# Kernel tuning notes

Measured on AMD Instinct MI355X. Metric: run time of the kernel, lower is better.

The kernel has to match this reference:

```python
import jax, jax.numpy as jnp
import numpy as np

P = 7          # output_size
SR = 2         # sampling_ratio
SCALES = (0.25, 0.125, 0.0625, 0.03125)
K_MIN, K_MAX = 2.0, 5.0   # -log2(max scale), -log2(min scale)
LVL0, S0, EPS = 4.0, 224.0, 1e-6  # torchvision LevelMapper defaults


def _coverage(x1, x2, size):
    """Fractional per-pixel coverage of interval [x1, x2] along an axis.
    Reproduces fill_masks_for_boxes edge weighting. x1, x2: [K] -> [K, size]."""
    cols = jnp.arange(size, dtype=x1.dtype)[None, :]
    x1f = jnp.floor(x1)[:, None]
    x2c = jnp.ceil(x2)[:, None]
    inside = ((cols >= x1f) & (cols < x2c)).astype(x1.dtype)
    wl = jnp.where(cols == x1f, 1.0 + x1f - x1[:, None], 1.0)
    wr = jnp.where(cols == x2c - 1.0, 1.0 + x2[:, None] - x2c, 1.0)
    return inside * wl * wr


def _axis_interp(coord, size):
    """torchvision roi_align (aligned=False) 1D bilinear setup.
    Returns lo/hi indices and weights (zeroed for out-of-range points)."""
    valid = ((coord >= -1.0) & (coord <= size)).astype(coord.dtype)
    c = jnp.maximum(coord, 0.0)
    lo0 = jnp.floor(c)
    top = lo0 >= size - 1
    lo = jnp.where(top, float(size - 1), lo0)
    hi = jnp.where(top, float(size - 1), lo0 + 1.0)
    c = jnp.where(top, float(size - 1), c)
    frac = c - lo
    return lo.astype(jnp.int32), hi.astype(jnp.int32), (1.0 - frac) * valid, frac * valid


def _level_roi(feat, scale, ub, bo, bidx):
    """Masked RoIAlign of the union box over one pyramid level.
    feat: [N,C,H,W]; ub, bo: [K,4] image-coord boxes; bidx: [K] int32."""
    N, C, H, W = feat.shape
    K = ub.shape[0]
    ubs = ub * scale
    bos = bo * scale

    def clipb(b):
        return (jnp.clip(b[:, 0], 0.0, W), jnp.clip(b[:, 1], 0.0, H),
                jnp.clip(b[:, 2], 0.0, W), jnp.clip(b[:, 3], 0.0, H))

    ux1, uy1, ux2, uy2 = clipb(ubs)
    ox1, oy1, ox2, oy2 = clipb(bos)
    # Separable pair-mask coverage (NOTE: torch code mutates boxes_h into the
    # union in-place before mask construction, so the 'h' mask is the union mask).
    cxu = _coverage(ux1, ux2, W)  # [K,W]
    cyu = _coverage(uy1, uy2, H)  # [K,H]
    cxo = _coverage(ox1, ox2, W)
    cyo = _coverage(oy1, oy2, H)

    x1, y1, x2, y2 = ubs[:, 0], ubs[:, 1], ubs[:, 2], ubs[:, 3]
    roi_w = jnp.maximum(x2 - x1, 1.0)
    roi_h = jnp.maximum(y2 - y1, 1.0)
    i = jnp.arange(P * SR)
    t = (i // SR).astype(jnp.float32) + ((i % SR).astype(jnp.float32) + 0.5) / SR  # bin units
    px = x1[:, None] + t[None, :] * (roi_w / P)[:, None]  # [K, P*SR]
    py = y1[:, None] + t[None, :] * (roi_h / P)[:, None]
    xlo, xhi, wxl, wxh = _axis_interp(px, W)
    ylo, yhi, wyl, wyh = _axis_interp(py, H)

    ga = lambda tab, idx: jnp.take_along_axis(tab, idx, axis=1)
    ys, wy = (ylo, yhi), (wyl, wyh)
    xs, wx = (xlo, xhi), (wxl, wxh)
    myu = (ga(cyu, ylo), ga(cyu, yhi))
    mxu = (ga(cxu, xlo), ga(cxu, xhi))
    myo = (ga(cyo, ylo), ga(cyo, yhi))
    mxo = (ga(cxo, xlo), ga(cxo, xhi))

    acc = jnp.zeros((K, P * SR, P * SR, C), dtype=feat.dtype)
    for a in range(2):
        for b in range(2):
            # gather corner features: [K, Ps, Ps, C]
            fv = feat[bidx[:, None, None], :, ys[a][:, :, None], xs[b][:, None, :]]
            m = jnp.maximum(myu[a][:, :, None] * mxu[b][:, None, :],
                            myo[a][:, :, None] * mxo[b][:, None, :])
            wgt = wy[a][:, :, None] * wx[b][:, None, :] * m
            acc = acc + wgt[..., None] * fv
    out = acc.reshape(K, P, SR, P, SR, C).mean(axis=(2, 4))  # avg over sample grid
    return jnp.transpose(out, (0, 3, 1, 2))  # [K, C, P, P]


def _forward(feat0, feat1, feat2, feat3, boxes_h, boxes_o):
    feats = (feat0, feat1, feat2, feat3)
    bidx = boxes_h[:, 0].astype(jnp.int32)
    bh = boxes_h[:, 1:]
    bo = boxes_o[:, 1:]
    ub = jnp.stack([jnp.minimum(bh[:, 0], bo[:, 0]), jnp.minimum(bh[:, 1], bo[:, 1]),
                    jnp.maximum(bh[:, 2], bo[:, 2]), jnp.maximum(bh[:, 3], bo[:, 3])], axis=1)
    # Level mapping (boxes_h already mutated into the union in the torch code)
    su = jnp.sqrt((ub[:, 2] - ub[:, 0]) * (ub[:, 3] - ub[:, 1]))
    so = jnp.sqrt((bo[:, 2] - bo[:, 0]) * (bo[:, 3] - bo[:, 1]))
    s = jnp.minimum(su, so)
    lv = (jnp.clip(jnp.floor(LVL0 + jnp.log2(s / S0 + EPS)), K_MIN, K_MAX)).astype(jnp.int32) - int(K_MIN)
    K, C = boxes_h.shape[0], feat0.shape[1]
    out = jnp.zeros((K, C, P, P), dtype=feat0.dtype)
    for l, (f, sc) in enumerate(zip(feats, SCALES)):
        ol = _level_roi(f, sc, ub, bo, bidx)
        out = out + jnp.where((lv == l)[:, None, None, None], ol, 0.0)
    return out


def setup_inputs() -> dict:
    key = jax.random.key(0)
    ks = jax.random.split(key, 12)
    feat0 = jax.random.normal(ks[0], (2, 256, 128, 128), dtype=jnp.float32)
    feat1 = jax.random.normal(ks[1], (2, 256, 64, 64), dtype=jnp.float32)
    feat2 = jax.random.normal(ks[2], (2, 256, 32, 32), dtype=jnp.float32)
    feat3 = jax.random.normal(ks[3], (2, 256, 16, 16), dtype=jnp.float32)
    K = 512
    bidx = jax.random.randint(ks[4], (K,), 0, 2).astype(jnp.float32)

    def mk(k):
        k1, k2, k3, k4 = jax.random.split(k, 4)
        x1 = jax.random.uniform(k1, (K,), minval=0.0, maxval=112.0)
        y1 = jax.random.uniform(k2, (K,), minval=0.0, maxval=112.0)
        w = jax.random.uniform(k3, (K,), minval=16.0, maxval=400.0)
        h = jax.random.uniform(k4, (K,), minval=16.0, maxval=400.0)
        return jnp.stack([bidx, x1, y1, x1 + w, y1 + h], axis=1)  # image is 512x512

    return {"feat0": feat0, "feat1": feat1, "feat2": feat2, "feat3": feat3,
            "boxes_h": mk(ks[5]), "boxes_o": mk(ks[6])}


def reference(feat0, feat1, feat2, feat3, boxes_h, boxes_o):
    return _forward(feat0, feat1, feat2, feat3, boxes_h, boxes_o)
```

## Files before the change

kernel.cpp:

```cpp
#include <hip/hip_runtime.h>
#include <math.h>

#define PP 7
#define CCH 256

__device__ __forceinline__ float coverage(float colf, float a, float b) {
    float af = floorf(a);
    float bc = ceilf(b);
    float v  = (colf >= af && colf < bc) ? 1.0f : 0.0f;
    float wl = (colf == af) ? (1.0f + af - a) : 1.0f;
    float wr = (colf == bc - 1.0f) ? (1.0f + b - bc) : 1.0f;
    return v * wl * wr;
}

__global__ __launch_bounds__(256) void nchw_to_nhwc_all(
    const float* __restrict__ f0, const float* __restrict__ f1,
    const float* __restrict__ f2, const float* __restrict__ f3,
    float* __restrict__ w0, float* __restrict__ w1,
    float* __restrict__ w2, float* __restrict__ w3, int NIMG)
{
    __shared__ float tile[64][65];
    int b = blockIdx.x;
    const float* src; float* dst; int HW, hw64;
    const int t0 = NIMG * 1024, t1 = t0 + NIMG * 256, t2 = t1 + NIMG * 64;
    if (b < t0)      {          src = f0; dst = w0; HW = 16384; hw64 = 256; }
    else if (b < t1) { b -= t0; src = f1; dst = w1; HW = 4096;  hw64 = 64;  }
    else if (b < t2) { b -= t1; src = f2; dst = w2; HW = 1024;  hw64 = 16;  }
    else             { b -= t2; src = f3; dst = w3; HW = 256;   hw64 = 4;   }
    const int tpi  = hw64 * 4;
    const int n    = b / tpi;
    const int r    = b - n * tpi;
    const int cb   = r / hw64;
    const int pix0 = (r - cb * hw64) * 64;
    const int c0   = cb * 64;

    const int tx = threadIdx.x & 63, ty = threadIdx.x >> 6;
    const float* s = src + ((size_t)n * CCH + c0) * HW + pix0;
    #pragma unroll
    for (int i = 0; i < 16; ++i) {
        const int rr = i*4 + ty;
        tile[rr][tx] = s[(size_t)rr * HW + tx];
    }
    __syncthreads();
    float* d = dst + ((size_t)n * HW + pix0) * CCH + c0;
    #pragma unroll
    for (int i = 0; i < 16; ++i) {
        const int p = i*4 + ty;
        d[(size_t)p * CCH + tx] = tile[tx][p];
    }
}

__global__ __launch_bounds__(128) void roi_gather_nhwc(
    const float* __restrict__ n0, const float* __restrict__ n1,
    const float* __restrict__ n2, const float* __restrict__ n3,
    const float* __restrict__ bh, const float* __restrict__ bo,
    float* __restrict__ out, int K)
{
    const int k    = blockIdx.x;
    const int half = blockIdx.y;
    const int tid  = threadIdx.x;
    const int c    = half * 128 + tid;

    __shared__ int   t_xoff_lo[14], t_xoff_hi[14];
    __shared__ int   s_yoff_lo[14], s_yoff_hi[14];
    __shared__ float wbin[49][16];
    __shared__ float t_wxl[14], t_wxh[14], t_cxu0[14], t_cxu1[14], t_cxo0[14], t_cxo1[14];
    __shared__ float t_wyl[14], t_wyh[14], t_cyu0[14], t_cyu1[14], t_cyo0[14], t_cyo1[14];

    const float hx1 = bh[k*5+1], hy1 = bh[k*5+2], hx2 = bh[k*5+3], hy2 = bh[k*5+4];
    const float px1 = bo[k*5+1], py1 = bo[k*5+2], px2 = bo[k*5+3], py2 = bo[k*5+4];
    const int   bimg = (int)bh[k*5+0];

    const float ux1 = fminf(hx1, px1), uy1 = fminf(hy1, py1);
    const float ux2 = fmaxf(hx2, px2), uy2 = fmaxf(hy2, py2);
    const float su = sqrtf((ux2-ux1)*(uy2-uy1));
    const float so = sqrtf((px2-px1)*(py2-py1));
    const float s  = fminf(su, so);
    float lvf = floorf(4.0f + log2f(s/224.0f + 1e-6f));
    lvf = fminf(fmaxf(lvf, 2.0f), 5.0f);
    const int lv = (int)lvf - 2;

    const float scales[4] = {0.25f, 0.125f, 0.0625f, 0.03125f};
    const int   dims[4]   = {128, 64, 32, 16};
    const float scale = scales[lv];
    const int   W = dims[lv], H = W;
    const int   HW = W * H;
    const float Wf = (float)W, Hf = (float)H;
    const float* nh = (lv == 0) ? n0 : (lv == 1) ? n1 : (lv == 2) ? n2 : n3;

    const float usx1 = ux1*scale, usy1 = uy1*scale, usx2 = ux2*scale, usy2 = uy2*scale;
    const float osx1 = px1*scale, osy1 = py1*scale, osx2 = px2*scale, osy2 = py2*scale;
    const float cux1 = fminf(fmaxf(usx1, 0.f), Wf), cux2 = fminf(fmaxf(usx2, 0.f), Wf);
    const float cuy1 = fminf(fmaxf(usy1, 0.f), Hf), cuy2 = fminf(fmaxf(usy2, 0.f), Hf);
    const float cox1 = fminf(fmaxf(osx1, 0.f), Wf), cox2 = fminf(fmaxf(osx2, 0.f), Wf);
    const float coy1 = fminf(fmaxf(osy1, 0.f), Hf), coy2 = fminf(fmaxf(osy2, 0.f), Hf);
    const float roi_w = fmaxf(usx2 - usx1, 1.0f);
    const float roi_h = fmaxf(usy2 - usy1, 1.0f);

    if (tid < 14) {
        const int i = tid;
        const float t = (float)(i >> 1) + 0.25f + 0.5f*(float)(i & 1);
        const float p = usx1 + t * (roi_w / 7.0f);
        const float valid = (p >= -1.0f && p <= Wf) ? 1.0f : 0.0f;
        float cc = fmaxf(p, 0.0f);
        const float lo0 = floorf(cc);
        const bool top = (lo0 >= Wf - 1.0f);
        const float lo = top ? (Wf - 1.0f) : lo0;
        const float hi = top ? (Wf - 1.0f) : (lo0 + 1.0f);
        cc = top ? (Wf - 1.0f) : cc;
        const float frac = cc - lo;
        t_xoff_lo[i] = (int)lo * CCH;  t_xoff_hi[i] = (int)hi * CCH;
        t_wxl[i] = (1.0f - frac) * valid;  t_wxh[i] = frac * valid;
        t_cxu0[i] = coverage(lo, cux1, cux2);
        t_cxu1[i] = coverage(hi, cux1, cux2);
        t_cxo0[i] = coverage(lo, cox1, cox2);
        t_cxo1[i] = coverage(hi, cox1, cox2);
    } else if (tid >= 64 && tid < 78) {
        const int i = tid - 64;
        const float t = (float)(i >> 1) + 0.25f + 0.5f*(float)(i & 1);
        const float p = usy1 + t * (roi_h / 7.0f);
        const float valid = (p >= -1.0f && p <= Hf) ? 1.0f : 0.0f;
        float cc = fmaxf(p, 0.0f);
        const float lo0 = floorf(cc);
        const bool top = (lo0 >= Hf - 1.0f);
        const float lo = top ? (Hf - 1.0f) : lo0;
        const float hi = top ? (Hf - 1.0f) : (lo0 + 1.0f);
        cc = top ? (Hf - 1.0f) : cc;
        const float frac = cc - lo;
        s_yoff_lo[i] = (int)lo * W * CCH;  s_yoff_hi[i] = (int)hi * W * CCH;
        t_wyl[i] = (1.0f - frac) * valid;  t_wyh[i] = frac * valid;
        t_cyu0[i] = coverage(lo, cuy1, cuy2);
        t_cyu1[i] = coverage(hi, cuy1, cuy2);
        t_cyo0[i] = coverage(lo, coy1, coy2);
        t_cyo1[i] = coverage(hi, coy1, coy2);
    }
    __syncthreads();

    if (tid < 49) {
        const int bpy = tid / 7, bpx = tid - bpy * 7;
        #pragma unroll
        for (int isy = 0; isy < 2; ++isy) {
            const int sy = 2*bpy + isy;
            const float wy0 = t_wyl[sy], wy1 = t_wyh[sy];
            const float yu0 = t_cyu0[sy], yu1 = t_cyu1[sy];
            const float yo0 = t_cyo0[sy], yo1 = t_cyo1[sy];
            #pragma unroll
            for (int isx = 0; isx < 2; ++isx) {
                const int sxm = 2*bpx + isx;
                const float wx0 = t_wxl[sxm], wx1 = t_wxh[sxm];
                const float xu0 = t_cxu0[sxm], xu1 = t_cxu1[sxm];
                const float xo0 = t_cxo0[sxm], xo1 = t_cxo1[sxm];
                const int p4 = (isy*2 + isx) * 4;
                wbin[tid][p4+0] = wy0*wx0*fmaxf(yu0*xu0, yo0*xo0);
                wbin[tid][p4+1] = wy0*wx1*fmaxf(yu0*xu1, yo0*xo1);
                wbin[tid][p4+2] = wy1*wx0*fmaxf(yu1*xu0, yo1*xo0);
                wbin[tid][p4+3] = wy1*wx1*fmaxf(yu1*xu1, yo1*xo1);
            }
        }
    }
    __syncthreads();

    const float* pb = nh + (size_t)bimg * HW * CCH + c;
    float* okc = out + (size_t)k * (CCH * PP * PP) + (size_t)c * (PP * PP);

    for (int pyy = 0; pyy < 7; ++pyy) {
        float accs[7] = {0,0,0,0,0,0,0};
        #pragma unroll
        for (int isy = 0; isy < 2; ++isy) {
            const int sy  = 2*pyy + isy;
            const int yoL = s_yoff_lo[sy], yoH = s_yoff_hi[sy];
            #pragma unroll
            for (int ix = 0; ix < 14; ++ix) {
                const int pxb = ix >> 1, isx = ix & 1;
                const float4 w = *(const float4*)&wbin[pyy*7 + pxb][(isy*2 + isx)*4];
                const int xoL = t_xoff_lo[ix], xoH = t_xoff_hi[ix];
                accs[pxb] += w.x*pb[yoL + xoL] + w.y*pb[yoL + xoH]
                           + w.z*pb[yoH + xoL] + w.w*pb[yoH + xoH];
            }
        }
        float* op = okc + pyy * PP;
        #pragma unroll
        for (int q = 0; q < 7; ++q) op[q] = accs[q] * 0.25f;
    }
}

__global__ __launch_bounds__(256) void roi_pair_kernel(
    const float* __restrict__ f0, const float* __restrict__ f1,
    const float* __restrict__ f2, const float* __restrict__ f3,
    const float* __restrict__ bh, const float* __restrict__ bo,
    float* __restrict__ out, int K)
{
    const int k  = blockIdx.x;
    const int py = blockIdx.y;
    const int c  = threadIdx.x;

    __shared__ int   t_xlo[14], t_xhi[14];
    __shared__ float t_wxl[14], t_wxh[14], t_cxu0[14], t_cxu1[14], t_cxo0[14], t_cxo1[14];
    __shared__ int   s_ylo[2], s_yhi[2];
    __shared__ float s_wyl[2], s_wyh[2], s_cyu0[2], s_cyu1[2], s_cyo0[2], s_cyo1[2];

    const float hx1 = bh[k*5+1], hy1 = bh[k*5+2], hx2 = bh[k*5+3], hy2 = bh[k*5+4];
    const float px1 = bo[k*5+1], py1 = bo[k*5+2], px2 = bo[k*5+3], py2 = bo[k*5+4];
    const int   bimg = (int)bh[k*5+0];

    const float ux1 = fminf(hx1, px1), uy1 = fminf(hy1, py1);
    const float ux2 = fmaxf(hx2, px2), uy2 = fmaxf(hy2, py2);
    const float su = sqrtf((ux2-ux1)*(uy2-uy1));
    const float so = sqrtf((px2-px1)*(py2-py1));
    const float s  = fminf(su, so);
    float lvf = floorf(4.0f + log2f(s/224.0f + 1e-6f));
    lvf = fminf(fmaxf(lvf, 2.0f), 5.0f);
    const int lv = (int)lvf - 2;

    const float scales[4] = {0.25f, 0.125f, 0.0625f, 0.03125f};
    const int   dims[4]   = {128, 64, 32, 16};
    const float scale = scales[lv];
    const int   W = dims[lv], H = W;
    const float Wf = (float)W, Hf = (float)H;
    const float* feat = (lv == 0) ? f0 : (lv == 1) ? f1 : (lv == 2) ? f2 : f3;

    const float usx1 = ux1*scale, usy1 = uy1*scale, usx2 = ux2*scale, usy2 = uy2*scale;
    const float osx1 = px1*scale, osy1 = py1*scale, osx2 = px2*scale, osy2 = py2*scale;
    const float cux1 = fminf(fmaxf(usx1, 0.f), Wf), cux2 = fminf(fmaxf(usx2, 0.f), Wf);
    const float cuy1 = fminf(fmaxf(usy1, 0.f), Hf), cuy2 = fminf(fmaxf(usy2, 0.f), Hf);
    const float cox1 = fminf(fmaxf(osx1, 0.f), Wf), cox2 = fminf(fmaxf(osx2, 0.f), Wf);
    const float coy1 = fminf(fmaxf(osy1, 0.f), Hf), coy2 = fminf(fmaxf(osy2, 0.f), Hf);
    const float roi_w = fmaxf(usx2 - usx1, 1.0f);
    const float roi_h = fmaxf(usy2 - usy1, 1.0f);

    if (threadIdx.x < 14) {
        const int i = threadIdx.x;
        const float t = (float)(i >> 1) + 0.25f + 0.5f*(float)(i & 1);
        const float p = usx1 + t * (roi_w / 7.0f);
        const float valid = (p >= -1.0f && p <= Wf) ? 1.0f : 0.0f;
        float cc = fmaxf(p, 0.0f);
        const float lo0 = floorf(cc);
        const bool top = (lo0 >= Wf - 1.0f);
        const float lo = top ? (Wf - 1.0f) : lo0;
        const float hi = top ? (Wf - 1.0f) : (lo0 + 1.0f);
        cc = top ? (Wf - 1.0f) : cc;
        const float frac = cc - lo;
        t_xlo[i] = (int)lo;  t_xhi[i] = (int)hi;
        t_wxl[i] = (1.0f - frac) * valid;  t_wxh[i] = frac * valid;
        t_cxu0[i] = coverage(lo, cux1, cux2);
        t_cxu1[i] = coverage(hi, cux1, cux2);
        t_cxo0[i] = coverage(lo, cox1, cox2);
        t_cxo1[i] = coverage(hi, cox1, cox2);
    } else if (threadIdx.x >= 64 && threadIdx.x < 66) {
        const int isy = threadIdx.x - 64;
        const int i = 2*py + isy;
        const float t = (float)(i >> 1) + 0.25f + 0.5f*(float)(i & 1);
        const float p = usy1 + t * (roi_h / 7.0f);
        const float valid = (p >= -1.0f && p <= Hf) ? 1.0f : 0.0f;
        float cc = fmaxf(p, 0.0f);
        const float lo0 = floorf(cc);
        const bool top = (lo0 >= Hf - 1.0f);
        const float lo = top ? (Hf - 1.0f) : lo0;
        const float hi = top ? (Hf - 1.0f) : (lo0 + 1.0f);
        cc = top ? (Hf - 1.0f) : cc;
        const float frac = cc - lo;
        s_ylo[isy] = (int)lo;  s_yhi[isy] = (int)hi;
        s_wyl[isy] = (1.0f - frac) * valid;  s_wyh[isy] = frac * valid;
        s_cyu0[isy] = coverage(lo, cuy1, cuy2);
        s_cyu1[isy] = coverage(hi, cuy1, cuy2);
        s_cyo0[isy] = coverage(lo, coy1, coy2);
        s_cyo1[isy] = coverage(hi, coy1, coy2);
    }
    __syncthreads();

    const float* fc = feat + (size_t)(bimg * CCH + c) * (H * W);
    float accs[7] = {0,0,0,0,0,0,0};

    #pragma unroll
    for (int isy = 0; isy < 2; ++isy) {
        const int   ylo = s_ylo[isy], yhi = s_yhi[isy];
        const float wyl = s_wyl[isy], wyh = s_wyh[isy];
        const float cyu0 = s_cyu0[isy], cyu1 = s_cyu1[isy];
        const float cyo0 = s_cyo0[isy], cyo1 = s_cyo1[isy];
        const float* rlo = fc + ylo * W;
        const float* rhi = fc + yhi * W;
        #pragma unroll
        for (int ix = 0; ix < 14; ++ix) {
            const int pxb = ix >> 1;
            const int xlo = t_xlo[ix], xhi = t_xhi[ix];
            const float wxl = t_wxl[ix], wxh = t_wxh[ix];
            const float cxu0 = t_cxu0[ix], cxu1 = t_cxu1[ix];
            const float cxo0 = t_cxo0[ix], cxo1 = t_cxo1[ix];
            const float w00 = wyl*wxl*fmaxf(cyu0*cxu0, cyo0*cxo0);
            const float w01 = wyl*wxh*fmaxf(cyu0*cxu1, cyo0*cxo1);
            const float w10 = wyh*wxl*fmaxf(cyu1*cxu0, cyo1*cxo0);
            const float w11 = wyh*wxh*fmaxf(cyu1*cxu1, cyo1*cxo1);
            accs[pxb] += w00*rlo[xlo] + w01*rlo[xhi] + w10*rhi[xlo] + w11*rhi[xhi];
        }
    }

    float* op = out + ((size_t)k * CCH + c) * (PP * PP) + py * PP;
    #pragma unroll
    for (int pxb = 0; pxb < 7; ++pxb) op[pxb] = accs[pxb] * 0.25f;
}

extern "C" void kernel_launch(void* const* d_in, const int* in_sizes, int n_in,
                              void* d_out, int out_size, void* d_ws, size_t ws_size,
                              hipStream_t stream) {
    const float* f0 = (const float*)d_in[0];
    const float* f1 = (const float*)d_in[1];
    const float* f2 = (const float*)d_in[2];
    const float* f3 = (const float*)d_in[3];
    const float* bh = (const float*)d_in[4];
    const float* bo = (const float*)d_in[5];
    float* out = (float*)d_out;
    const int K = in_sizes[4] / 5;
    const int NIMG = in_sizes[0] / (CCH * 128 * 128);

    const size_t hw0 = 128*128, hw1 = 64*64, hw2 = 32*32, hw3 = 16*16;
    const size_t sz0 = (size_t)NIMG * CCH * hw0;
    const size_t sz1 = (size_t)NIMG * CCH * hw1;
    const size_t sz2 = (size_t)NIMG * CCH * hw2;
    const size_t sz3 = (size_t)NIMG * CCH * hw3;
    const size_t need_bytes = (sz0 + sz1 + sz2 + sz3) * sizeof(float);

    if (ws_size >= need_bytes) {
        float* w0 = (float*)d_ws;
        float* w1 = w0 + sz0;
        float* w2 = w1 + sz1;
        float* w3 = w2 + sz2;

        const int tiles = NIMG * (1024 + 256 + 64 + 16);
        nchw_to_nhwc_all<<<tiles, 256, 0, stream>>>(f0, f1, f2, f3, w0, w1, w2, w3, NIMG);
        roi_gather_nhwc<<<dim3(K, 2), 128, 0, stream>>>(w0, w1, w2, w3, bh, bo, out, K);
    } else {
        roi_pair_kernel<<<dim3(K, PP), CCH, 0, stream>>>(f0, f1, f2, f3, bh, bo, out, K);
    }
}
```

Baseline: 146.6 us.

## Restructure RoI gather: one block per RoI, float4 channel loads, LDS-staged coalesced output

The gather kernel now runs one 448-thread block per RoI instead of two 128-thread blocks. Each of the 7 wavefronts handles one output row, and each lane loads four consecutive channels with float4 reads from the NHWC feature map. Results are transposed through a 50 KB shared-memory stage so global stores are fully coalesced, replacing the previous stride-49 per-channel writes. The trade-off is lower occupancy from the large LDS footprint and more registers per thread.

```diff
diff --git a/kernel.cpp b/kernel.cpp
--- a/kernel.cpp
+++ b/kernel.cpp
@@ -50,20 +50,21 @@
     }
 }
 
-__global__ __launch_bounds__(128) void roi_gather_nhwc(
+__global__ __launch_bounds__(448) void roi_gather_nhwc(
     const float* __restrict__ n0, const float* __restrict__ n1,
     const float* __restrict__ n2, const float* __restrict__ n3,
     const float* __restrict__ bh, const float* __restrict__ bo,
     float* __restrict__ out, int K)
 {
     const int k    = blockIdx.x;
-    const int half = blockIdx.y;
     const int tid  = threadIdx.x;
-    const int c    = half * 128 + tid;
-
+    const int wpy  = tid >> 6;
+    const int lane = tid & 63;
+
+    __shared__ float stage[CCH * 49];
+    __shared__ float wbin[49][16];
     __shared__ int   t_xoff_lo[14], t_xoff_hi[14];
     __shared__ int   s_yoff_lo[14], s_yoff_hi[14];
-    __shared__ float wbin[49][16];
     __shared__ float t_wxl[14], t_wxh[14], t_cxu0[14], t_cxu1[14], t_cxo0[14], t_cxo1[14];
     __shared__ float t_wyl[14], t_wyh[14], t_cyu0[14], t_cyu1[14], t_cyo0[14], t_cyo1[14];
 
@@ -160,27 +161,50 @@
     }
     __syncthreads();
 
-    const float* pb = nh + (size_t)bimg * HW * CCH + c;
-    float* okc = out + (size_t)k * (CCH * PP * PP) + (size_t)c * (PP * PP);
-
-    for (int pyy = 0; pyy < 7; ++pyy) {
-        float accs[7] = {0,0,0,0,0,0,0};
+    const float* pb = nh + (size_t)bimg * HW * CCH + 4*lane;
+
+    float4 acc[7];
+    #pragma unroll
+    for (int q = 0; q < 7; ++q) acc[q] = make_float4(0.f, 0.f, 0.f, 0.f);
+
+    #pragma unroll
+    for (int isy = 0; isy < 2; ++isy) {
+        const int sy  = 2*wpy + isy;
+        const int yoL = s_yoff_lo[sy], yoH = s_yoff_hi[sy];
         #pragma unroll
-        for (int isy = 0; isy < 2; ++isy) {
-            const int sy  = 2*pyy + isy;
-            const int yoL = s_yoff_lo[sy], yoH = s_yoff_hi[sy];
-            #pragma unroll
-            for (int ix = 0; ix < 14; ++ix) {
-                const int pxb = ix >> 1, isx = ix & 1;
-                const float4 w = *(const float4*)&wbin[pyy*7 + pxb][(isy*2 + isx)*4];
-                const int xoL = t_xoff_lo[ix], xoH = t_xoff_hi[ix];
-                accs[pxb] += w.x*pb[yoL + xoL] + w.y*pb[yoL + xoH]
-                           + w.z*pb[yoH + xoL] + w.w*pb[yoH + xoH];
-            }
+        for (int ix = 0; ix < 14; ++ix) {
+            const int pxb = ix >> 1, isx = ix & 1;
+            const float4 w = *(const float4*)&wbin[wpy*7 + pxb][(isy*2 + isx)*4];
+            const int xoL = t_xoff_lo[ix], xoH = t_xoff_hi[ix];
+            const float4 vLL = *(const float4*)(pb + yoL + xoL);
+            const float4 vLH = *(const float4*)(pb + yoL + xoH);
+            const float4 vHL = *(const float4*)(pb + yoH + xoL);
+            const float4 vHH = *(const float4*)(pb + yoH + xoH);
+            acc[pxb].x += w.x*vLL.x + w.y*vLH.x + w.z*vHL.x + w.w*vHH.x;
+            acc[pxb].y += w.x*vLL.y + w.y*vLH.y + w.z*vHL.y + w.w*vHH.y;
+            acc[pxb].z += w.x*vLL.z + w.y*vLH.z + w.z*vHL.z + w.w*vHH.z;
+            acc[pxb].w += w.x*vLL.w + w.y*vLH.w + w.z*vHL.w + w.w*vHH.w;
         }
-        float* op = okc + pyy * PP;
+    }
+
+    {
+        const int c0 = 4*lane;
         #pragma unroll
-        for (int q = 0; q < 7; ++q) op[q] = accs[q] * 0.25f;
+        for (int q = 0; q < 7; ++q) {
+            const int col = wpy*7 + q;
+            stage[(c0+0)*49 + col] = acc[q].x * 0.25f;
+            stage[(c0+1)*49 + col] = acc[q].y * 0.25f;
+            stage[(c0+2)*49 + col] = acc[q].z * 0.25f;
+            stage[(c0+3)*49 + col] = acc[q].w * 0.25f;
+        }
+    }
+    __syncthreads();
+
+    float* ok = out + (size_t)k * (CCH * 49);
+    #pragma unroll
+    for (int i = 0; i < 28; ++i) {
+        const int idx = tid + i*448;
+        ok[idx] = stage[idx];
     }
 }
 
@@ -327,7 +351,7 @@
 
         const int tiles = NIMG * (1024 + 256 + 64 + 16);
         nchw_to_nhwc_all<<<tiles, 256, 0, stream>>>(f0, f1, f2, f3, w0, w1, w2, w3, NIMG);
-        roi_gather_nhwc<<<dim3(K, 2), 128, 0, stream>>>(w0, w1, w2, w3, bh, bo, out, K);
+        roi_gather_nhwc<<<K, 448, 0, stream>>>(w0, w1, w2, w3, bh, bo, out, K);
     } else {
         roi_pair_kernel<<<dim3(K, PP), CCH, 0, stream>>>(f0, f1, f2, f3, bh, bo, out, K);
     }
```

New measurement: 130.9 us. 1.12x faster.
